# Optimization experiments

Measured on AMD Instinct MI355X. Metric: run time of the kernel, lower is better.

The kernel has to match this reference:

```python
import jax, jax.numpy as jnp
import numpy as np

N_NODES = 100000
N_EDGES = 3200000
N_GRAPHS = 1000

def setup_inputs() -> dict:
    key = jax.random.key(0)
    ks = jax.random.split(key, 8)
    x = jax.random.normal(ks[0], (N_NODES, 4), dtype=jnp.float32)
    edge_index = jax.random.randint(ks[1], (2, N_EDGES), 0, N_NODES, dtype=jnp.int64)
    batch = jnp.sort(jax.random.randint(ks[2], (N_NODES,), 0, N_GRAPHS, dtype=jnp.int64))
    def glorot(k, shape):
        lim = np.sqrt(6.0 / (shape[0] + shape[1]))
        return jax.random.uniform(k, shape, jnp.float32, -lim, lim)
    return {
        'x': x, 'edge_index': edge_index, 'batch': batch,
        'W1': glorot(ks[3], (4, 16)),  'b1': jnp.zeros((16,), jnp.float32),
        'W2': glorot(ks[4], (16, 16)), 'b2': jnp.zeros((16,), jnp.float32),
        'W3': glorot(ks[5], (16, 16)), 'b3': jnp.zeros((16,), jnp.float32),
        'lin_w': glorot(ks[6], (16, 1)), 'lin_b': jnp.zeros((1,), jnp.float32),
    }

def _gcn_norm(edge_index, num_nodes):
    # PyG GCNConv default: add self-loops, symmetric normalization
    loop = jnp.arange(num_nodes, dtype=edge_index.dtype)
    row = jnp.concatenate([edge_index[0], loop])  # source
    col = jnp.concatenate([edge_index[1], loop])  # target
    ones = jnp.ones(row.shape[0], dtype=jnp.float32)
    deg = jax.ops.segment_sum(ones, col, num_segments=num_nodes)
    dinv = jnp.where(deg > 0, jax.lax.rsqrt(deg), 0.0)
    norm = dinv[row] * dinv[col]  # [E+N]
    return row, col, norm

def _gcn_conv(x, row, col, norm, W, b, num_nodes):
    h = x @ W                                   # small GEMM first (fewer msg bytes)
    msg = h[row] * norm[:, None]                # gather + scale
    out = jax.ops.segment_sum(msg, col, num_segments=num_nodes)  # scatter-add
    return out + b

def reference(x, edge_index, batch, W1, b1, W2, b2, W3, b3, lin_w, lin_b):
    n = x.shape[0]
    row, col, norm = _gcn_norm(edge_index, n)
    h = _gcn_conv(x, row, col, norm, W1, b1, n)
    h = _gcn_conv(h, row, col, norm, W2, b2, n)
    h = _gcn_conv(h, row, col, norm, W3, b3, n)
    # global_mean_pool
    sums = jax.ops.segment_sum(h, batch, num_segments=N_GRAPHS)
    cnt = jax.ops.segment_sum(jnp.ones((n,), jnp.float32), batch, num_segments=N_GRAPHS)
    pooled = sums / jnp.maximum(cnt, 1.0)[:, None]
    # dropout p=0.5 is identity in eval mode
    logits = pooled @ lin_w + lin_b
    return jax.nn.sigmoid(logits)
```

## Files before the change

kernel.cpp:

```cpp
#include <hip/hip_runtime.h>
#include <math.h>


#define SHIFT      8
#define BSZ        256
#define NB_SCAT    256
#define SCAN_CHUNK 2048
#define PNODES     1024
#define ROWMASK    0x1FFFFu

__global__ void coeffs_kernel(const float* __restrict__ W1, const float* __restrict__ b1,
                              const float* __restrict__ W2, const float* __restrict__ b2,
                              const float* __restrict__ W3, const float* __restrict__ b3,
                              const float* __restrict__ lin_w, const float* __restrict__ lin_b,
                              float* __restrict__ coeff) {
    if (threadIdx.x == 0 && blockIdx.x == 0) {
        float w3l[16], w2l[16];
        for (int i = 0; i < 16; ++i) {
            float s = 0.f;
            for (int j = 0; j < 16; ++j) s += W3[i * 16 + j] * lin_w[j];
            w3l[i] = s;
        }
        for (int i = 0; i < 16; ++i) {
            float s = 0.f;
            for (int j = 0; j < 16; ++j) s += W2[i * 16 + j] * w3l[j];
            w2l[i] = s;
        }
        for (int i = 0; i < 4; ++i) {
            float s = 0.f;
            for (int j = 0; j < 16; ++j) s += W1[i * 16 + j] * w2l[j];
            coeff[i] = s;
        }
        float s2 = 0.f, s1 = 0.f, s0 = 0.f;
        for (int j = 0; j < 16; ++j) {
            s2 += b1[j] * w2l[j];
            s1 += b2[j] * w3l[j];
            s0 += b3[j] * lin_w[j];
        }
        coeff[4] = s2; coeff[5] = s1; coeff[6] = s0; coeff[7] = lin_b[0];
    }
}

__global__ void zero_pool_kernel(float* __restrict__ sums, float* __restrict__ cnt, int ngraphs) {
    int i = blockIdx.x * blockDim.x + threadIdx.x;
    if (i < ngraphs) { sums[i] = 0.f; cnt[i] = 0.f; }
}

__global__ void hist_kernel(const int* __restrict__ col, int E, int tile, int nbuck,
                            unsigned* __restrict__ M) {
    extern __shared__ unsigned h[];
    for (int i = threadIdx.x; i < nbuck; i += blockDim.x) h[i] = 0;
    __syncthreads();
    int b = blockIdx.x;
    int s = b * tile, e = min(s + tile, E);
    if (s < e) {
        int nq = (e - s) >> 2;
        const int4* c4 = (const int4*)(col + s);
        for (int q = threadIdx.x; q < nq; q += blockDim.x) {
            int4 c = c4[q];
            atomicAdd(&h[((unsigned)c.x) >> SHIFT], 1u);
            atomicAdd(&h[((unsigned)c.y) >> SHIFT], 1u);
            atomicAdd(&h[((unsigned)c.z) >> SHIFT], 1u);
            atomicAdd(&h[((unsigned)c.w) >> SHIFT], 1u);
        }
        for (int k = s + (nq << 2) + threadIdx.x; k < e; k += blockDim.x)
            atomicAdd(&h[((unsigned)col[k]) >> SHIFT], 1u);
    }
    __syncthreads();
    for (int i = threadIdx.x; i < nbuck; i += blockDim.x)
        M[(size_t)i * NB_SCAT + b] = h[i];
}

__global__ void scan1_kernel(const unsigned* __restrict__ M, unsigned* __restrict__ part,
                             int total, int chunk) {
    __shared__ unsigned sdata[256];
    int b = blockIdx.x;
    int s = b * chunk, e = min(s + chunk, total);
    unsigned sum = 0;
    for (int k = s + threadIdx.x; k < e; k += blockDim.x) sum += M[k];
    sdata[threadIdx.x] = sum;
    __syncthreads();
    for (int off = 128; off > 0; off >>= 1) {
        if (threadIdx.x < off) sdata[threadIdx.x] += sdata[threadIdx.x + off];
        __syncthreads();
    }
    if (threadIdx.x == 0) part[b] = sdata[0];
}

__global__ void scan2_kernel(unsigned* __restrict__ part, int np) {
    if (threadIdx.x == 0 && blockIdx.x == 0) {
        unsigned run = 0;
        for (int i = 0; i < np; ++i) { unsigned v = part[i]; part[i] = run; run += v; }
    }
}

__global__ void scan3_kernel(unsigned* __restrict__ M, const unsigned* __restrict__ part,
                             int total, int chunk) {
    __shared__ unsigned ts[256];
    int b = blockIdx.x;
    int s = b * chunk;
    const int per = SCAN_CHUNK / 256;
    unsigned v[per];
    unsigned sum = 0;
    int base = s + threadIdx.x * per;
    for (int j = 0; j < per; ++j) {
        unsigned x = (base + j < total) ? M[base + j] : 0u;
        v[j] = sum; sum += x;
    }
    ts[threadIdx.x] = sum;
    __syncthreads();
    for (int off = 1; off < 256; off <<= 1) {
        unsigned t = (threadIdx.x >= (unsigned)off) ? ts[threadIdx.x - off] : 0u;
        __syncthreads();
        ts[threadIdx.x] += t;
        __syncthreads();
    }
    unsigned texcl = (threadIdx.x == 0) ? 0u : ts[threadIdx.x - 1];
    unsigned pb = part[b];
    for (int j = 0; j < per; ++j)
        if (base + j < total) M[base + j] = pb + texcl + v[j];
}

__global__ void scatter_kernel(const int* __restrict__ row, const int* __restrict__ col,
                               int E, int tile, int nbuck, const unsigned* __restrict__ M,
                               unsigned* __restrict__ out) {
    extern __shared__ unsigned base[];
    int b = blockIdx.x;
    for (int i = threadIdx.x; i < nbuck; i += blockDim.x)
        base[i] = M[(size_t)i * NB_SCAT + b];
    __syncthreads();
    int s = b * tile, e = min(s + tile, E);
    if (s < e) {
        int nq = (e - s) >> 2;
        const int4* r4 = (const int4*)(row + s);
        const int4* c4 = (const int4*)(col + s);
        for (int q = threadIdx.x; q < nq; q += blockDim.x) {
            int4 r = r4[q];
            int4 c = c4[q];
            unsigned p0 = atomicAdd(&base[((unsigned)c.x) >> SHIFT], 1u);
            unsigned p1 = atomicAdd(&base[((unsigned)c.y) >> SHIFT], 1u);
            unsigned p2 = atomicAdd(&base[((unsigned)c.z) >> SHIFT], 1u);
            unsigned p3 = atomicAdd(&base[((unsigned)c.w) >> SHIFT], 1u);
            out[p0] = (unsigned)r.x | (((unsigned)c.x & (BSZ - 1)) << 17);
            out[p1] = (unsigned)r.y | (((unsigned)c.y & (BSZ - 1)) << 17);
            out[p2] = (unsigned)r.z | (((unsigned)c.z & (BSZ - 1)) << 17);
            out[p3] = (unsigned)r.w | (((unsigned)c.w & (BSZ - 1)) << 17);
        }
        for (int k = s + (nq << 2) + threadIdx.x; k < e; k += blockDim.x) {
            unsigned c = (unsigned)col[k];
            unsigned pos = atomicAdd(&base[c >> SHIFT], 1u);
            out[pos] = (unsigned)row[k] | ((c & (BSZ - 1)) << 17);
        }
    }
}

__global__ void deg0_kernel(const unsigned* __restrict__ buck, const unsigned* __restrict__ M,
                            int nbuck, int E, const float* __restrict__ x,
                            const float* __restrict__ coeff, float* __restrict__ dinv,
                            float* __restrict__ g, int n) {
    __shared__ float acc[BSZ];
    int b = blockIdx.x;
    acc[threadIdx.x] = 0.f;
    __syncthreads();
    unsigned s = M[(size_t)b * NB_SCAT];
    unsigned e = (b + 1 < nbuck) ? M[(size_t)(b + 1) * NB_SCAT] : (unsigned)E;
    unsigned sa = (s + 3u) & ~3u;
    if (sa > e) sa = e;
    if (s + threadIdx.x < sa)
        atomicAdd(&acc[buck[s + threadIdx.x] >> 17], 1.0f);
    unsigned nq = (e - sa) >> 2;
    const uint4* bq = (const uint4*)(buck + sa);
    for (unsigned q = threadIdx.x; q < nq; q += blockDim.x) {
        uint4 w = bq[q];
        atomicAdd(&acc[w.x >> 17], 1.0f);
        atomicAdd(&acc[w.y >> 17], 1.0f);
        atomicAdd(&acc[w.z >> 17], 1.0f);
        atomicAdd(&acc[w.w >> 17], 1.0f);
    }
    for (unsigned k = sa + (nq << 2) + threadIdx.x; k < e; k += blockDim.x)
        atomicAdd(&acc[buck[k] >> 17], 1.0f);
    __syncthreads();
    int node = b * BSZ + threadIdx.x;
    if (node < n) {
        float d = rsqrtf(acc[threadIdx.x] + 1.0f);
        dinv[node] = d;
        float4 xv = ((const float4*)x)[node];
        float t0 = xv.x * coeff[0] + xv.y * coeff[1] + xv.z * coeff[2] + xv.w * coeff[3];
        g[node] = d * t0;
    }
}

__global__ void gather_kernel(const unsigned* __restrict__ buck, const unsigned* __restrict__ M,
                              int nbuck, int E, const float* __restrict__ dinv,
                              const float* __restrict__ gin, float* __restrict__ gout,
                              const float* __restrict__ coeff, int sidx, int n, int lastPass) {
    __shared__ float acc[BSZ];
    int b = blockIdx.x;
    acc[threadIdx.x] = 0.f;
    __syncthreads();
    unsigned s = M[(size_t)b * NB_SCAT];
    unsigned e = (b + 1 < nbuck) ? M[(size_t)(b + 1) * NB_SCAT] : (unsigned)E;
    unsigned sa = (s + 3u) & ~3u;
    if (sa > e) sa = e;
    if (s + threadIdx.x < sa) {
        unsigned w = buck[s + threadIdx.x];
        atomicAdd(&acc[w >> 17], gin[w & ROWMASK]);
    }
    unsigned nq = (e - sa) >> 2;
    const uint4* bq = (const uint4*)(buck + sa);
    for (unsigned q = threadIdx.x; q < nq; q += blockDim.x) {
        uint4 w = bq[q];
        float a0 = gin[w.x & ROWMASK];
        float a1 = gin[w.y & ROWMASK];
        float a2 = gin[w.z & ROWMASK];
        float a3 = gin[w.w & ROWMASK];
        atomicAdd(&acc[w.x >> 17], a0);
        atomicAdd(&acc[w.y >> 17], a1);
        atomicAdd(&acc[w.z >> 17], a2);
        atomicAdd(&acc[w.w >> 17], a3);
    }
    for (unsigned k = sa + (nq << 2) + threadIdx.x; k < e; k += blockDim.x) {
        unsigned w = buck[k];
        atomicAdd(&acc[w >> 17], gin[w & ROWMASK]);
    }
    __syncthreads();
    int node = b * BSZ + threadIdx.x;
    if (node < n) {
        float d = dinv[node];
        float t = d * (acc[threadIdx.x] + gin[node]) + coeff[sidx];
        gout[node] = lastPass ? t : d * t;
    }
}

__global__ void pool_kernel(const float* __restrict__ t3, const int* __restrict__ batch,
                            float* __restrict__ sums, float* __restrict__ cnt, int n) {
    __shared__ float ls[1024];
    __shared__ float lc[1024];
    int s = blockIdx.x * PNODES, e = min(s + PNODES, n);
    if (s >= e) return;
    int bFirst = batch[s];
    int bLast  = batch[e - 1];
    int range = bLast - bFirst + 1;
    if (range <= 1024) {
        for (int i = threadIdx.x; i < range; i += blockDim.x) { ls[i] = 0.f; lc[i] = 0.f; }
        __syncthreads();
        for (int k = s + threadIdx.x; k < e; k += blockDim.x) {
            int bb = batch[k] - bFirst;
            atomicAdd(&ls[bb], t3[k]);
            atomicAdd(&lc[bb], 1.0f);
        }
        __syncthreads();
        for (int i = threadIdx.x; i < range; i += blockDim.x) {
            if (lc[i] != 0.f) {
                atomicAdd(&sums[bFirst + i], ls[i]);
                atomicAdd(&cnt[bFirst + i], lc[i]);
            }
        }
    } else {
        for (int k = s + threadIdx.x; k < e; k += blockDim.x) {
            atomicAdd(&sums[batch[k]], t3[k]);
            atomicAdd(&cnt[batch[k]], 1.0f);
        }
    }
}

__global__ void final_kernel(const float* __restrict__ sums, const float* __restrict__ cnt,
                             const float* __restrict__ coeff, float* __restrict__ out,
                             int ngraphs) {
    int i = blockIdx.x * blockDim.x + threadIdx.x;
    if (i < ngraphs) {
        float m = sums[i] / fmaxf(cnt[i], 1.0f) + coeff[7];
        out[i] = 1.0f / (1.0f + expf(-m));
    }
}

__global__ void fb_init_kernel(float* __restrict__ deg, float* __restrict__ sums,
                               float* __restrict__ cnt, int n, int ngraphs) {
    int i = blockIdx.x * blockDim.x + threadIdx.x;
    int stride = gridDim.x * blockDim.x;
    for (int k = i; k < n; k += stride) deg[k] = 1.0f;
    for (int k = i; k < ngraphs; k += stride) { sums[k] = 0.f; cnt[k] = 0.f; }
}
__global__ void fb_deg_kernel(const int* __restrict__ col, float* __restrict__ deg, int E) {
    int i = blockIdx.x * blockDim.x + threadIdx.x;
    int stride = gridDim.x * blockDim.x;
    for (int k = i; k < E; k += stride) atomicAdd(&deg[col[k]], 1.0f);
}
__global__ void fb_node0_kernel(const float* __restrict__ x, const float* __restrict__ coeff,
                                float* __restrict__ deg_dinv, float* __restrict__ g,
                                float* __restrict__ acc, int n) {
    int i = blockIdx.x * blockDim.x + threadIdx.x;
    int stride = gridDim.x * blockDim.x;
    for (int k = i; k < n; k += stride) {
        float d = rsqrtf(deg_dinv[k]);
        deg_dinv[k] = d;
        float4 xv = ((const float4*)x)[k];
        float t0 = xv.x * coeff[0] + xv.y * coeff[1] + xv.z * coeff[2] + xv.w * coeff[3];
        g[k] = d * t0;
        acc[k] = 0.f;
    }
}
__global__ void fb_edge_kernel(const int* __restrict__ ei, const float* __restrict__ g,
                               float* __restrict__ acc, int E) {
    int i = blockIdx.x * blockDim.x + threadIdx.x;
    int stride = gridDim.x * blockDim.x;
    for (int k = i; k < E; k += stride) atomicAdd(&acc[ei[E + k]], g[ei[k]]);
}
__global__ void fb_node_kernel(const float* __restrict__ dinv, float* __restrict__ g,
                               float* __restrict__ acc, const float* __restrict__ coeff,
                               int sidx, int n) {
    int i = blockIdx.x * blockDim.x + threadIdx.x;
    int stride = gridDim.x * blockDim.x;
    for (int k = i; k < n; k += stride) {
        float d = dinv[k];
        float t = d * (acc[k] + g[k]) + coeff[sidx];
        g[k] = d * t;
        acc[k] = 0.f;
    }
}
__global__ void fb_pool_kernel(const float* __restrict__ dinv, const float* __restrict__ g,
                               const float* __restrict__ acc, const float* __restrict__ coeff,
                               const int* __restrict__ batch, float* __restrict__ sums,
                               float* __restrict__ cnt, int n) {
    int i = blockIdx.x * blockDim.x + threadIdx.x;
    int stride = gridDim.x * blockDim.x;
    for (int k = i; k < n; k += stride) {
        float d = dinv[k];
        float t3 = d * (acc[k] + g[k]) + coeff[6];
        int b = batch[k];
        atomicAdd(&sums[b], t3);
        atomicAdd(&cnt[b], 1.0f);
    }
}

extern "C" void kernel_launch(void* const* d_in, const int* in_sizes, int n_in,
                              void* d_out, int out_size, void* d_ws, size_t ws_size,
                              hipStream_t stream) {
    const float* x     = (const float*)d_in[0];
    const int*   ei    = (const int*)d_in[1];
    const int*   batch = (const int*)d_in[2];
    const float* W1    = (const float*)d_in[3];
    const float* b1    = (const float*)d_in[4];
    const float* W2    = (const float*)d_in[5];
    const float* b2    = (const float*)d_in[6];
    const float* W3    = (const float*)d_in[7];
    const float* b3    = (const float*)d_in[8];
    const float* lin_w = (const float*)d_in[9];
    const float* lin_b = (const float*)d_in[10];

    const int n       = in_sizes[0] / 4;
    const int E       = in_sizes[1] / 2;
    const int ngraphs = out_size;

    const int nbuck = (n + BSZ - 1) / BSZ;
    const int B = 256;

    size_t npad = ((size_t)n + 255) & ~(size_t)255;
    size_t gpad = ((size_t)ngraphs + 255) & ~(size_t)255;
    size_t mlen = (size_t)nbuck * NB_SCAT;
    int total   = (int)mlen;
    int nchunks = (total + SCAN_CHUNK - 1) / SCAN_CHUNK;

    size_t need = (256 + mlen + 1024 + (size_t)E + 3 * npad + 2 * gpad) * 4;

    float* ws   = (float*)d_ws;
    float* coeff = ws;
    unsigned* M    = (unsigned*)(coeff + 256);
    unsigned* part = M + mlen;
    unsigned* buck = part + 1024;
    float* dinv  = (float*)(buck + E);
    float* gA    = dinv + npad;
    float* gB    = gA + npad;
    float* sums  = gB + npad;
    float* cnt   = sums + gpad;

    coeffs_kernel<<<1, 64, 0, stream>>>(W1, b1, W2, b2, W3, b3, lin_w, lin_b, coeff);

    if (ws_size < need) {
        float* deg = (float*)(ws + 256);
        float* g   = deg + npad;
        float* acc = g + npad;
        float* fsums = acc + npad;
        float* fcnt  = fsums + gpad;
        int nodeBlocks = (n + B - 1) / B;
        int edgeBlocks = (E + B - 1) / B;
        fb_init_kernel<<<nodeBlocks, B, 0, stream>>>(deg, fsums, fcnt, n, ngraphs);
        fb_deg_kernel<<<edgeBlocks, B, 0, stream>>>(ei + E, deg, E);
        fb_node0_kernel<<<nodeBlocks, B, 0, stream>>>(x, coeff, deg, g, acc, n);
        fb_edge_kernel<<<edgeBlocks, B, 0, stream>>>(ei, g, acc, E);
        fb_node_kernel<<<nodeBlocks, B, 0, stream>>>(deg, g, acc, coeff, 4, n);
        fb_edge_kernel<<<edgeBlocks, B, 0, stream>>>(ei, g, acc, E);
        fb_node_kernel<<<nodeBlocks, B, 0, stream>>>(deg, g, acc, coeff, 5, n);
        fb_edge_kernel<<<edgeBlocks, B, 0, stream>>>(ei, g, acc, E);
        fb_pool_kernel<<<nodeBlocks, B, 0, stream>>>(deg, g, acc, coeff, batch, fsums, fcnt, n);
        final_kernel<<<(ngraphs + B - 1) / B, B, 0, stream>>>(fsums, fcnt, coeff, (float*)d_out, ngraphs);
        return;
    }

    int tile = (((E + NB_SCAT - 1) / NB_SCAT) + 3) & ~3;
    size_t ldsHist = (size_t)nbuck * sizeof(unsigned);

    zero_pool_kernel<<<(ngraphs + B - 1) / B, B, 0, stream>>>(sums, cnt, ngraphs);

    hist_kernel<<<NB_SCAT, B, ldsHist, stream>>>(ei + E, E, tile, nbuck, M);
    scan1_kernel<<<nchunks, B, 0, stream>>>(M, part, total, SCAN_CHUNK);
    scan2_kernel<<<1, 64, 0, stream>>>(part, nchunks);
    scan3_kernel<<<nchunks, B, 0, stream>>>(M, part, total, SCAN_CHUNK);
    scatter_kernel<<<NB_SCAT, B, ldsHist, stream>>>(ei, ei + E, E, tile, nbuck, M, buck);

    deg0_kernel<<<nbuck, B, 0, stream>>>(buck, M, nbuck, E, x, coeff, dinv, gA, n);

    gather_kernel<<<nbuck, B, 0, stream>>>(buck, M, nbuck, E, dinv, gA, gB, coeff, 4, n, 0);
    gather_kernel<<<nbuck, B, 0, stream>>>(buck, M, nbuck, E, dinv, gB, gA, coeff, 5, n, 0);
    gather_kernel<<<nbuck, B, 0, stream>>>(buck, M, nbuck, E, dinv, gA, gB, coeff, 6, n, 1);

    pool_kernel<<<(n + PNODES - 1) / PNODES, B, 0, stream>>>(gB, batch, sums, cnt, n);

    final_kernel<<<(ngraphs + B - 1) / B, B, 0, stream>>>(sums, cnt, coeff, (float*)d_out, ngraphs);
}
```

Measured before the change: 157.8 us.

## Fuse setup kernels, restructure bucket scan, halve bucket size, fuse pooling into gather

```diff
diff --git a/kernel.cpp b/kernel.cpp
--- a/kernel.cpp
+++ b/kernel.cpp
@@ -2,139 +2,145 @@
 #include <math.h>
 
 
-#define SHIFT      8
-#define BSZ        256
+#define SHIFT      7
+#define BSZ        128
 #define NB_SCAT    256
-#define SCAN_CHUNK 2048
-#define PNODES     1024
 #define ROWMASK    0x1FFFFu
-
-__global__ void coeffs_kernel(const float* __restrict__ W1, const float* __restrict__ b1,
-                              const float* __restrict__ W2, const float* __restrict__ b2,
-                              const float* __restrict__ W3, const float* __restrict__ b3,
-                              const float* __restrict__ lin_w, const float* __restrict__ lin_b,
-                              float* __restrict__ coeff) {
-    if (threadIdx.x == 0 && blockIdx.x == 0) {
-        float w3l[16], w2l[16];
-        for (int i = 0; i < 16; ++i) {
-            float s = 0.f;
-            for (int j = 0; j < 16; ++j) s += W3[i * 16 + j] * lin_w[j];
-            w3l[i] = s;
-        }
-        for (int i = 0; i < 16; ++i) {
-            float s = 0.f;
-            for (int j = 0; j < 16; ++j) s += W2[i * 16 + j] * w3l[j];
-            w2l[i] = s;
-        }
-        for (int i = 0; i < 4; ++i) {
-            float s = 0.f;
-            for (int j = 0; j < 16; ++j) s += W1[i * 16 + j] * w2l[j];
-            coeff[i] = s;
-        }
-        float s2 = 0.f, s1 = 0.f, s0 = 0.f;
-        for (int j = 0; j < 16; ++j) {
-            s2 += b1[j] * w2l[j];
-            s1 += b2[j] * w3l[j];
-            s0 += b3[j] * lin_w[j];
-        }
-        coeff[4] = s2; coeff[5] = s1; coeff[6] = s0; coeff[7] = lin_b[0];
-    }
-}
-
-__global__ void zero_pool_kernel(float* __restrict__ sums, float* __restrict__ cnt, int ngraphs) {
-    int i = blockIdx.x * blockDim.x + threadIdx.x;
-    if (i < ngraphs) { sums[i] = 0.f; cnt[i] = 0.f; }
-}
+#define PSLOTS     64
 
 __global__ void hist_kernel(const int* __restrict__ col, int E, int tile, int nbuck,
-                            unsigned* __restrict__ M) {
+                            unsigned* __restrict__ M,
+                            const float* __restrict__ W1, const float* __restrict__ b1,
+                            const float* __restrict__ W2, const float* __restrict__ b2,
+                            const float* __restrict__ W3, const float* __restrict__ b3,
+                            const float* __restrict__ lin_w, const float* __restrict__ lin_b,
+                            float* __restrict__ coeff,
+                            float* __restrict__ sums, float* __restrict__ cnt, int ngraphs) {
     extern __shared__ unsigned h[];
-    for (int i = threadIdx.x; i < nbuck; i += blockDim.x) h[i] = 0;
-    __syncthreads();
+    __shared__ float w3l[16], w2l[16];
+    int t = threadIdx.x;
+    for (int i = t; i < nbuck; i += blockDim.x) h[i] = 0;
+    if (blockIdx.x == 0) {
+        for (int i = t; i < ngraphs; i += blockDim.x) { sums[i] = 0.f; cnt[i] = 0.f; }
+        if (t < 16) {
+            float s = 0.f;
+            for (int j = 0; j < 16; ++j) s += W3[t * 16 + j] * lin_w[j];
+            w3l[t] = s;
+        }
+    }
+    __syncthreads();
+    if (blockIdx.x == 0 && t < 16) {
+        float s = 0.f;
+        for (int j = 0; j < 16; ++j) s += W2[t * 16 + j] * w3l[j];
+        w2l[t] = s;
+    }
+    __syncthreads();
+    if (blockIdx.x == 0) {
+        if (t < 4) {
+            float s = 0.f;
+            for (int j = 0; j < 16; ++j) s += W1[t * 16 + j] * w2l[j];
+            coeff[t] = s;
+        } else if (t == 4) {
+            float s = 0.f;
+            for (int j = 0; j < 16; ++j) s += b1[j] * w2l[j];
+            coeff[4] = s;
+        } else if (t == 5) {
+            float s = 0.f;
+            for (int j = 0; j < 16; ++j) s += b2[j] * w3l[j];
+            coeff[5] = s;
+        } else if (t == 6) {
+            float s = 0.f;
+            for (int j = 0; j < 16; ++j) s += b3[j] * lin_w[j];
+            coeff[6] = s;
+        } else if (t == 7) {
+            coeff[7] = lin_b[0];
+        }
+    }
     int b = blockIdx.x;
     int s = b * tile, e = min(s + tile, E);
     if (s < e) {
         int nq = (e - s) >> 2;
         const int4* c4 = (const int4*)(col + s);
-        for (int q = threadIdx.x; q < nq; q += blockDim.x) {
+        for (int q = t; q < nq; q += blockDim.x) {
             int4 c = c4[q];
             atomicAdd(&h[((unsigned)c.x) >> SHIFT], 1u);
             atomicAdd(&h[((unsigned)c.y) >> SHIFT], 1u);
             atomicAdd(&h[((unsigned)c.z) >> SHIFT], 1u);
             atomicAdd(&h[((unsigned)c.w) >> SHIFT], 1u);
         }
-        for (int k = s + (nq << 2) + threadIdx.x; k < e; k += blockDim.x)
+        for (int k = s + (nq << 2) + t; k < e; k += blockDim.x)
             atomicAdd(&h[((unsigned)col[k]) >> SHIFT], 1u);
     }
     __syncthreads();
-    for (int i = threadIdx.x; i < nbuck; i += blockDim.x)
-        M[(size_t)i * NB_SCAT + b] = h[i];
-}
-
-__global__ void scan1_kernel(const unsigned* __restrict__ M, unsigned* __restrict__ part,
-                             int total, int chunk) {
-    __shared__ unsigned sdata[256];
+    for (int i = t; i < nbuck; i += blockDim.x)
+        M[(size_t)b * nbuck + i] = h[i];
+}
+
+__global__ void scanA_kernel(unsigned* __restrict__ M, unsigned* __restrict__ binTotal,
+                             int nbuck) {
+    __shared__ unsigned sc[NB_SCAT];
     int b = blockIdx.x;
-    int s = b * chunk, e = min(s + chunk, total);
-    unsigned sum = 0;
-    for (int k = s + threadIdx.x; k < e; k += blockDim.x) sum += M[k];
-    sdata[threadIdx.x] = sum;
-    __syncthreads();
-    for (int off = 128; off > 0; off >>= 1) {
-        if (threadIdx.x < off) sdata[threadIdx.x] += sdata[threadIdx.x + off];
+    int t = threadIdx.x;
+    unsigned v = M[(size_t)t * nbuck + b];
+    sc[t] = v;
+    __syncthreads();
+    for (int off = 1; off < NB_SCAT; off <<= 1) {
+        unsigned u = (t >= off) ? sc[t - off] : 0u;
         __syncthreads();
-    }
-    if (threadIdx.x == 0) part[b] = sdata[0];
-}
-
-__global__ void scan2_kernel(unsigned* __restrict__ part, int np) {
-    if (threadIdx.x == 0 && blockIdx.x == 0) {
-        unsigned run = 0;
-        for (int i = 0; i < np; ++i) { unsigned v = part[i]; part[i] = run; run += v; }
-    }
-}
-
-__global__ void scan3_kernel(unsigned* __restrict__ M, const unsigned* __restrict__ part,
-                             int total, int chunk) {
-    __shared__ unsigned ts[256];
-    int b = blockIdx.x;
-    int s = b * chunk;
-    const int per = SCAN_CHUNK / 256;
-    unsigned v[per];
-    unsigned sum = 0;
-    int base = s + threadIdx.x * per;
-    for (int j = 0; j < per; ++j) {
-        unsigned x = (base + j < total) ? M[base + j] : 0u;
-        v[j] = sum; sum += x;
-    }
-    ts[threadIdx.x] = sum;
-    __syncthreads();
-    for (int off = 1; off < 256; off <<= 1) {
-        unsigned t = (threadIdx.x >= (unsigned)off) ? ts[threadIdx.x - off] : 0u;
+        sc[t] += u;
         __syncthreads();
-        ts[threadIdx.x] += t;
+    }
+    M[(size_t)t * nbuck + b] = sc[t] - v;
+    if (t == NB_SCAT - 1) binTotal[b] = sc[t];
+}
+
+__global__ void scatter_kernel(const int* __restrict__ row, const int* __restrict__ col,
+                               int E, int tile, int nbuck,
+                               const unsigned* __restrict__ M,
+                               const unsigned* __restrict__ binTotal,
+                               unsigned* __restrict__ bstart,
+                               unsigned* __restrict__ out) {
+    extern __shared__ unsigned lds[];
+    unsigned* bb   = lds;
+    unsigned* base = lds + nbuck;
+    unsigned* tsum = lds + 2 * nbuck;
+    int t = threadIdx.x;
+    int C = (nbuck + NB_SCAT - 1) >> 8;
+    unsigned lv[8];
+    unsigned ls = 0;
+    for (int k = 0; k < C; ++k) {
+        int i = t * C + k;
+        unsigned x = (i < nbuck) ? binTotal[i] : 0u;
+        lv[k] = ls; ls += x;
+    }
+    tsum[t] = ls;
+    __syncthreads();
+    for (int off = 1; off < NB_SCAT; off <<= 1) {
+        unsigned u = (t >= off) ? tsum[t - off] : 0u;
         __syncthreads();
-    }
-    unsigned texcl = (threadIdx.x == 0) ? 0u : ts[threadIdx.x - 1];
-    unsigned pb = part[b];
-    for (int j = 0; j < per; ++j)
-        if (base + j < total) M[base + j] = pb + texcl + v[j];
-}
-
-__global__ void scatter_kernel(const int* __restrict__ row, const int* __restrict__ col,
-                               int E, int tile, int nbuck, const unsigned* __restrict__ M,
-                               unsigned* __restrict__ out) {
-    extern __shared__ unsigned base[];
-    int b = blockIdx.x;
-    for (int i = threadIdx.x; i < nbuck; i += blockDim.x)
-        base[i] = M[(size_t)i * NB_SCAT + b];
-    __syncthreads();
-    int s = b * tile, e = min(s + tile, E);
+        tsum[t] += u;
+        __syncthreads();
+    }
+    unsigned ex = (t == 0) ? 0u : tsum[t - 1];
+    for (int k = 0; k < C; ++k) {
+        int i = t * C + k;
+        if (i < nbuck) bb[i] = ex + lv[k];
+    }
+    __syncthreads();
+    int j = blockIdx.x;
+    for (int i = t; i < nbuck; i += blockDim.x)
+        base[i] = bb[i] + M[(size_t)j * nbuck + i];
+    if (j == 0) {
+        for (int i = t; i < nbuck; i += blockDim.x) bstart[i] = bb[i];
+        if (t == 0) bstart[nbuck] = (unsigned)E;
+    }
+    __syncthreads();
+    int s = j * tile, e = min(s + tile, E);
     if (s < e) {
         int nq = (e - s) >> 2;
         const int4* r4 = (const int4*)(row + s);
         const int4* c4 = (const int4*)(col + s);
-        for (int q = threadIdx.x; q < nq; q += blockDim.x) {
+        for (int q = t; q < nq; q += blockDim.x) {
             int4 r = r4[q];
             int4 c = c4[q];
             unsigned p0 = atomicAdd(&base[((unsigned)c.x) >> SHIFT], 1u);
@@ -146,7 +152,7 @@
             out[p2] = (unsigned)r.z | (((unsigned)c.z & (BSZ - 1)) << 17);
             out[p3] = (unsigned)r.w | (((unsigned)c.w & (BSZ - 1)) << 17);
         }
-        for (int k = s + (nq << 2) + threadIdx.x; k < e; k += blockDim.x) {
+        for (int k = s + (nq << 2) + t; k < e; k += blockDim.x) {
             unsigned c = (unsigned)col[k];
             unsigned pos = atomicAdd(&base[c >> SHIFT], 1u);
             out[pos] = (unsigned)row[k] | ((c & (BSZ - 1)) << 17);
@@ -154,16 +160,15 @@
     }
 }
 
-__global__ void deg0_kernel(const unsigned* __restrict__ buck, const unsigned* __restrict__ M,
-                            int nbuck, int E, const float* __restrict__ x,
-                            const float* __restrict__ coeff, float* __restrict__ dinv,
-                            float* __restrict__ g, int n) {
+__global__ void degnode0_kernel(const unsigned* __restrict__ buck,
+                                const unsigned* __restrict__ bstart,
+                                const float* __restrict__ x, const float* __restrict__ coeff,
+                                float* __restrict__ dinv, float* __restrict__ g, int n) {
     __shared__ float acc[BSZ];
     int b = blockIdx.x;
     acc[threadIdx.x] = 0.f;
     __syncthreads();
-    unsigned s = M[(size_t)b * NB_SCAT];
-    unsigned e = (b + 1 < nbuck) ? M[(size_t)(b + 1) * NB_SCAT] : (unsigned)E;
+    unsigned s = bstart[b], e = bstart[b + 1];
     unsigned sa = (s + 3u) & ~3u;
     if (sa > e) sa = e;
     if (s + threadIdx.x < sa)
@@ -190,16 +195,16 @@
     }
 }
 
-__global__ void gather_kernel(const unsigned* __restrict__ buck, const unsigned* __restrict__ M,
-                              int nbuck, int E, const float* __restrict__ dinv,
-                              const float* __restrict__ gin, float* __restrict__ gout,
-                              const float* __restrict__ coeff, int sidx, int n, int lastPass) {
+__global__ void gather_kernel(const unsigned* __restrict__ buck,
+                              const unsigned* __restrict__ bstart,
+                              const float* __restrict__ dinv, const float* __restrict__ gin,
+                              float* __restrict__ gout, const float* __restrict__ coeff,
+                              int sidx, int n) {
     __shared__ float acc[BSZ];
     int b = blockIdx.x;
     acc[threadIdx.x] = 0.f;
     __syncthreads();
-    unsigned s = M[(size_t)b * NB_SCAT];
-    unsigned e = (b + 1 < nbuck) ? M[(size_t)(b + 1) * NB_SCAT] : (unsigned)E;
+    unsigned s = bstart[b], e = bstart[b + 1];
     unsigned sa = (s + 3u) & ~3u;
     if (sa > e) sa = e;
     if (s + threadIdx.x < sa) {
@@ -228,38 +233,66 @@
     if (node < n) {
         float d = dinv[node];
         float t = d * (acc[threadIdx.x] + gin[node]) + coeff[sidx];
-        gout[node] = lastPass ? t : d * t;
-    }
-}
-
-__global__ void pool_kernel(const float* __restrict__ t3, const int* __restrict__ batch,
-                            float* __restrict__ sums, float* __restrict__ cnt, int n) {
-    __shared__ float ls[1024];
-    __shared__ float lc[1024];
-    int s = blockIdx.x * PNODES, e = min(s + PNODES, n);
-    if (s >= e) return;
-    int bFirst = batch[s];
-    int bLast  = batch[e - 1];
-    int range = bLast - bFirst + 1;
-    if (range <= 1024) {
-        for (int i = threadIdx.x; i < range; i += blockDim.x) { ls[i] = 0.f; lc[i] = 0.f; }
-        __syncthreads();
-        for (int k = s + threadIdx.x; k < e; k += blockDim.x) {
-            int bb = batch[k] - bFirst;
-            atomicAdd(&ls[bb], t3[k]);
-            atomicAdd(&lc[bb], 1.0f);
-        }
-        __syncthreads();
-        for (int i = threadIdx.x; i < range; i += blockDim.x) {
-            if (lc[i] != 0.f) {
-                atomicAdd(&sums[bFirst + i], ls[i]);
-                atomicAdd(&cnt[bFirst + i], lc[i]);
-            }
-        }
-    } else {
-        for (int k = s + threadIdx.x; k < e; k += blockDim.x) {
-            atomicAdd(&sums[batch[k]], t3[k]);
-            atomicAdd(&cnt[batch[k]], 1.0f);
+        gout[node] = d * t;
+    }
+}
+
+__global__ void gatherpool_kernel(const unsigned* __restrict__ buck,
+                                  const unsigned* __restrict__ bstart,
+                                  const float* __restrict__ dinv, const float* __restrict__ gin,
+                                  const float* __restrict__ coeff, const int* __restrict__ batch,
+                                  float* __restrict__ sums, float* __restrict__ cnt, int n) {
+    __shared__ float acc[BSZ];
+    __shared__ float ls[PSLOTS], lc[PSLOTS];
+    __shared__ int bF;
+    int b = blockIdx.x;
+    acc[threadIdx.x] = 0.f;
+    for (int i = threadIdx.x; i < PSLOTS; i += blockDim.x) { ls[i] = 0.f; lc[i] = 0.f; }
+    if (threadIdx.x == 0) bF = batch[b * BSZ];
+    __syncthreads();
+    unsigned s = bstart[b], e = bstart[b + 1];
+    unsigned sa = (s + 3u) & ~3u;
+    if (sa > e) sa = e;
+    if (s + threadIdx.x < sa) {
+        unsigned w = buck[s + threadIdx.x];
+        atomicAdd(&acc[w >> 17], gin[w & ROWMASK]);
+    }
+    unsigned nq = (e - sa) >> 2;
+    const uint4* bq = (const uint4*)(buck + sa);
+    for (unsigned q = threadIdx.x; q < nq; q += blockDim.x) {
+        uint4 w = bq[q];
+        float a0 = gin[w.x & ROWMASK];
+        float a1 = gin[w.y & ROWMASK];
+        float a2 = gin[w.z & ROWMASK];
+        float a3 = gin[w.w & ROWMASK];
+        atomicAdd(&acc[w.x >> 17], a0);
+        atomicAdd(&acc[w.y >> 17], a1);
+        atomicAdd(&acc[w.z >> 17], a2);
+        atomicAdd(&acc[w.w >> 17], a3);
+    }
+    for (unsigned k = sa + (nq << 2) + threadIdx.x; k < e; k += blockDim.x) {
+        unsigned w = buck[k];
+        atomicAdd(&acc[w >> 17], gin[w & ROWMASK]);
+    }
+    __syncthreads();
+    int node = b * BSZ + threadIdx.x;
+    if (node < n) {
+        float d = dinv[node];
+        float t3 = d * (acc[threadIdx.x] + gin[node]) + coeff[6];
+        int rb = batch[node] - bF;
+        if (rb < PSLOTS) {
+            atomicAdd(&ls[rb], t3);
+            atomicAdd(&lc[rb], 1.0f);
+        } else {
+            atomicAdd(&sums[bF + rb], t3);
+            atomicAdd(&cnt[bF + rb], 1.0f);
+        }
+    }
+    __syncthreads();
+    for (int i = threadIdx.x; i < PSLOTS; i += blockDim.x) {
+        if (lc[i] != 0.f) {
+            atomicAdd(&sums[bF + i], ls[i]);
+            atomicAdd(&cnt[bF + i], lc[i]);
         }
     }
 }
@@ -274,12 +307,43 @@
     }
 }
 
-__global__ void fb_init_kernel(float* __restrict__ deg, float* __restrict__ sums,
-                               float* __restrict__ cnt, int n, int ngraphs) {
+__global__ void fb_coeffs_kernel(const float* __restrict__ W1, const float* __restrict__ b1,
+                                 const float* __restrict__ W2, const float* __restrict__ b2,
+                                 const float* __restrict__ W3, const float* __restrict__ b3,
+                                 const float* __restrict__ lin_w, const float* __restrict__ lin_b,
+                                 float* __restrict__ coeff,
+                                 float* __restrict__ sums, float* __restrict__ cnt, int ngraphs) {
+    for (int i = threadIdx.x; i < ngraphs; i += blockDim.x) { sums[i] = 0.f; cnt[i] = 0.f; }
+    if (threadIdx.x == 0) {
+        float w3l[16], w2l[16];
+        for (int i = 0; i < 16; ++i) {
+            float s = 0.f;
+            for (int j = 0; j < 16; ++j) s += W3[i * 16 + j] * lin_w[j];
+            w3l[i] = s;
+        }
+        for (int i = 0; i < 16; ++i) {
+            float s = 0.f;
+            for (int j = 0; j < 16; ++j) s += W2[i * 16 + j] * w3l[j];
+            w2l[i] = s;
+        }
+        for (int i = 0; i < 4; ++i) {
+            float s = 0.f;
+            for (int j = 0; j < 16; ++j) s += W1[i * 16 + j] * w2l[j];
+            coeff[i] = s;
+        }
+        float s2 = 0.f, s1 = 0.f, s0 = 0.f;
+        for (int j = 0; j < 16; ++j) {
+            s2 += b1[j] * w2l[j];
+            s1 += b2[j] * w3l[j];
+            s0 += b3[j] * lin_w[j];
+        }
+        coeff[4] = s2; coeff[5] = s1; coeff[6] = s0; coeff[7] = lin_b[0];
+    }
+}
+__global__ void fb_init_kernel(float* __restrict__ deg, int n) {
     int i = blockIdx.x * blockDim.x + threadIdx.x;
     int stride = gridDim.x * blockDim.x;
     for (int k = i; k < n; k += stride) deg[k] = 1.0f;
-    for (int k = i; k < ngraphs; k += stride) { sums[k] = 0.f; cnt[k] = 0.f; }
 }
 __global__ void fb_deg_kernel(const int* __restrict__ col, float* __restrict__ deg, int E) {
     int i = blockIdx.x * blockDim.x + threadIdx.x;
@@ -355,66 +419,67 @@
     const int nbuck = (n + BSZ - 1) / BSZ;
     const int B = 256;
 
-    size_t npad = ((size_t)n + 255) & ~(size_t)255;
-    size_t gpad = ((size_t)ngraphs + 255) & ~(size_t)255;
-    size_t mlen = (size_t)nbuck * NB_SCAT;
-    int total   = (int)mlen;
-    int nchunks = (total + SCAN_CHUNK - 1) / SCAN_CHUNK;
-
-    size_t need = (256 + mlen + 1024 + (size_t)E + 3 * npad + 2 * gpad) * 4;
-
-    float* ws   = (float*)d_ws;
+    size_t npad  = ((size_t)n + 255) & ~(size_t)255;
+    size_t gpad  = ((size_t)ngraphs + 255) & ~(size_t)255;
+    size_t nbpad = ((size_t)nbuck + 1 + 255) & ~(size_t)255;
+    size_t mlen  = (size_t)NB_SCAT * nbuck;
+
+    size_t need = (256 + mlen + 2 * nbpad + (size_t)E + 3 * npad + 2 * gpad) * 4;
+
+    float* ws    = (float*)d_ws;
     float* coeff = ws;
-    unsigned* M    = (unsigned*)(coeff + 256);
-    unsigned* part = M + mlen;
-    unsigned* buck = part + 1024;
+    unsigned* M        = (unsigned*)(coeff + 256);
+    unsigned* binTotal = M + mlen;
+    unsigned* bstart   = binTotal + nbpad;
+    unsigned* buck     = bstart + nbpad;
     float* dinv  = (float*)(buck + E);
     float* gA    = dinv + npad;
     float* gB    = gA + npad;
     float* sums  = gB + npad;
     float* cnt   = sums + gpad;
 
-    coeffs_kernel<<<1, 64, 0, stream>>>(W1, b1, W2, b2, W3, b3, lin_w, lin_b, coeff);
-
-    if (ws_size < need) {
-        float* deg = (float*)(ws + 256);
+    bool mainok = (n < (1 << 17)) && nbuck >= 1 && nbuck <= 2048 && ws_size >= need;
+
+    if (!mainok) {
+        float* fcoeff = ws;
+        float* deg = fcoeff + 256;
         float* g   = deg + npad;
         float* acc = g + npad;
         float* fsums = acc + npad;
         float* fcnt  = fsums + gpad;
         int nodeBlocks = (n + B - 1) / B;
         int edgeBlocks = (E + B - 1) / B;
-        fb_init_kernel<<<nodeBlocks, B, 0, stream>>>(deg, fsums, fcnt, n, ngraphs);
+        fb_coeffs_kernel<<<1, 64, 0, stream>>>(W1, b1, W2, b2, W3, b3, lin_w, lin_b, fcoeff,
+                                               fsums, fcnt, ngraphs);
+        fb_init_kernel<<<nodeBlocks, B, 0, stream>>>(deg, n);
         fb_deg_kernel<<<edgeBlocks, B, 0, stream>>>(ei + E, deg, E);
-        fb_node0_kernel<<<nodeBlocks, B, 0, stream>>>(x, coeff, deg, g, acc, n);
+        fb_node0_kernel<<<nodeBlocks, B, 0, stream>>>(x, fcoeff, deg, g, acc, n);
         fb_edge_kernel<<<edgeBlocks, B, 0, stream>>>(ei, g, acc, E);
-        fb_node_kernel<<<nodeBlocks, B, 0, stream>>>(deg, g, acc, coeff, 4, n);
+        fb_node_kernel<<<nodeBlocks, B, 0, stream>>>(deg, g, acc, fcoeff, 4, n);
         fb_edge_kernel<<<edgeBlocks, B, 0, stream>>>(ei, g, acc, E);
-        fb_node_kernel<<<nodeBlocks, B, 0, stream>>>(deg, g, acc, coeff, 5, n);
+        fb_node_kernel<<<nodeBlocks, B, 0, stream>>>(deg, g, acc, fcoeff, 5, n);
         fb_edge_kernel<<<edgeBlocks, B, 0, stream>>>(ei, g, acc, E);
-        fb_pool_kernel<<<nodeBlocks, B, 0, stream>>>(deg, g, acc, coeff, batch, fsums, fcnt, n);
-        final_kernel<<<(ngraphs + B - 1) / B, B, 0, stream>>>(fsums, fcnt, coeff, (float*)d_out, ngraphs);
+        fb_pool_kernel<<<nodeBlocks, B, 0, stream>>>(deg, g, acc, fcoeff, batch, fsums, fcnt, n);
+        final_kernel<<<(ngraphs + B - 1) / B, B, 0, stream>>>(fsums, fcnt, fcoeff, (float*)d_out, ngraphs);
         return;
     }
 
     int tile = (((E + NB_SCAT - 1) / NB_SCAT) + 3) & ~3;
     size_t ldsHist = (size_t)nbuck * sizeof(unsigned);
-
-    zero_pool_kernel<<<(ngraphs + B - 1) / B, B, 0, stream>>>(sums, cnt, ngraphs);
-
-    hist_kernel<<<NB_SCAT, B, ldsHist, stream>>>(ei + E, E, tile, nbuck, M);
-    scan1_kernel<<<nchunks, B, 0, stream>>>(M, part, total, SCAN_CHUNK);
-    scan2_kernel<<<1, 64, 0, stream>>>(part, nchunks);
-    scan3_kernel<<<nchunks, B, 0, stream>>>(M, part, total, SCAN_CHUNK);
-    scatter_kernel<<<NB_SCAT, B, ldsHist, stream>>>(ei, ei + E, E, tile, nbuck, M, buck);
-
-    deg0_kernel<<<nbuck, B, 0, stream>>>(buck, M, nbuck, E, x, coeff, dinv, gA, n);
-
-    gather_kernel<<<nbuck, B, 0, stream>>>(buck, M, nbuck, E, dinv, gA, gB, coeff, 4, n, 0);
-    gather_kernel<<<nbuck, B, 0, stream>>>(buck, M, nbuck, E, dinv, gB, gA, coeff, 5, n, 0);
-    gather_kernel<<<nbuck, B, 0, stream>>>(buck, M, nbuck, E, dinv, gA, gB, coeff, 6, n, 1);
-
-    pool_kernel<<<(n + PNODES - 1) / PNODES, B, 0, stream>>>(gB, batch, sums, cnt, n);
+    size_t ldsScat = (size_t)(2 * nbuck + NB_SCAT) * sizeof(unsigned);
+
+    hist_kernel<<<NB_SCAT, B, ldsHist, stream>>>(ei + E, E, tile, nbuck, M,
+                                                 W1, b1, W2, b2, W3, b3, lin_w, lin_b,
+                                                 coeff, sums, cnt, ngraphs);
+    scanA_kernel<<<nbuck, NB_SCAT, 0, stream>>>(M, binTotal, nbuck);
+    scatter_kernel<<<NB_SCAT, B, ldsScat, stream>>>(ei, ei + E, E, tile, nbuck, M,
+                                                    binTotal, bstart, buck);
+
+    degnode0_kernel<<<nbuck, BSZ, 0, stream>>>(buck, bstart, x, coeff, dinv, gA, n);
+    gather_kernel<<<nbuck, BSZ, 0, stream>>>(buck, bstart, dinv, gA, gB, coeff, 4, n);
+    gather_kernel<<<nbuck, BSZ, 0, stream>>>(buck, bstart, dinv, gB, gA, coeff, 5, n);
+    gatherpool_kernel<<<nbuck, BSZ, 0, stream>>>(buck, bstart, dinv, gA, coeff, batch,
+                                                 sums, cnt, n);
 
     final_kernel<<<(ngraphs + B - 1) / B, B, 0, stream>>>(sums, cnt, coeff, (float*)d_out, ngraphs);
 }
```

New measurement: 144.4 us. 8.5% less time.
